# Kernel optimization log

Hardware: AMD Instinct MI355X
Metric: run time of the kernel (lower is better)

Reference implementation:

```python
import jax, jax.numpy as jnp
import numpy as np

B, K, N, D, E, EE, H, P = 512, 64, 1024, 128, 100000, 1024, 256, 12

def setup_inputs() -> dict:
    key = jax.random.key(0)
    ks = jax.random.split(key, 6)
    return {
        'ts_emb': jax.random.normal(ks[0], (B, D, N), jnp.float32),
        'event_table': jax.random.normal(ks[1], (E, EE), jnp.float32),
        'W_t': jax.random.normal(ks[2], (H, EE), jnp.float32) * 0.02,
        'b_t': jnp.zeros((H,), jnp.float32),
        'W_mm': jax.random.normal(ks[3], (P, H + D), jnp.float32) * 0.02,
        'b_mm': jnp.zeros((P,), jnp.float32),
        'W_ts': jax.random.normal(ks[4], (P, D), jnp.float32) * 0.02,
        'b_ts': jnp.zeros((P,), jnp.float32),
        'event_idx': jax.random.randint(ks[5], (B, K), 0, E, jnp.int64) if jax.config.read('jax_enable_x64') else jax.random.randint(ks[5], (B, K), 0, E, jnp.int32),
        'event_mask': jnp.ones((B, K), bool),
    }

def reference(ts_emb, event_table, W_t, b_t, W_mm, b_mm, W_ts, b_ts, event_idx, event_mask):
    h = W_t.shape[0]  # hidden_event_emb_dim
    # ragged event gather: [B, K, EE]
    ev = event_table[event_idx]
    # Linear(EE -> H): [B, K, H]
    ev_h = jnp.einsum('bke,he->bkh', ev, W_t) + b_t
    # masked max over events (event_fuse_type='max'): [B, H]
    neg = jnp.asarray(-jnp.inf, ev_h.dtype)
    ev_emb = jnp.max(jnp.where(event_mask[:, :, None], ev_h, neg), axis=1)
    # mm_forecaster = Conv1d(H+D -> P, k=1) on cat([event_emb repeat N, ts_emb]);
    # split the channel-wise linear so the broadcast part is never materialized.
    mm_ev = ev_emb @ W_mm[:, :h].T                       # [B, P]
    mm_ts = jnp.einsum('pd,bdn->bpn', W_mm[:, h:], ts_emb)  # [B, P, N]
    mm_pred = mm_ev[:, :, None] + mm_ts + b_mm[None, :, None]
    # ts_forecaster = Conv1d(D -> P, k=1)
    ts_pred = jnp.einsum('pd,bdn->bpn', W_ts, ts_emb) + b_ts[None, :, None]
    return (ts_pred + mm_pred) * 0.5
```

## Files before the change

### kernel.cpp

```cpp
#include <hip/hip_runtime.h>
#include <hip/hip_bf16.h>
#include <math.h>

#define B_   512
#define KEV  64
#define NN   1024
#define DD   128
#define EE_  1024
#define HH   256
#define PP   12
#define BK   128
#define NSTEP (EE_ / BK)

typedef __bf16 bf16x8 __attribute__((ext_vector_type(8)));
typedef float  f32x4  __attribute__((ext_vector_type(4)));
typedef unsigned short ushort8_t __attribute__((ext_vector_type(8)));

static __device__ __forceinline__ unsigned short f2bf(float f) {
    unsigned int u = __builtin_bit_cast(unsigned int, f);
    u = (u + 0x7FFFu + ((u >> 16) & 1u)) >> 16;
    return (unsigned short)u;
}

__global__ __launch_bounds__(256) void prep_kernel(
    const float* __restrict__ Wt,
    const float* __restrict__ Wmm,
    const float* __restrict__ Wts,
    const unsigned int* __restrict__ idxW,
    const unsigned int* __restrict__ mskW,
    unsigned short* __restrict__ WtBf,
    float* __restrict__ Wc,
    int* __restrict__ flags)
{
    if (blockIdx.x < 256) {
        int i4 = (blockIdx.x * 256 + threadIdx.x) * 4;
        const float4 v = *reinterpret_cast<const float4*>(Wt + i4);
        ushort4 o = make_ushort4(f2bf(v.x), f2bf(v.y), f2bf(v.z), f2bf(v.w));
        *reinterpret_cast<ushort4*>(WtBf + i4) = o;
        return;
    }
    __shared__ int any_nz;
    if (threadIdx.x == 0) any_nz = 0;
    __syncthreads();
    int local = 0;
    for (int k = threadIdx.x; k < (B_ * KEV) / 2; k += 256)
        local |= (idxW[2 * k + 1] != 0u);
    if (local) atomicOr(&any_nz, 1);
    for (int k = threadIdx.x; k < PP * DD; k += 256) {
        int p = k >> 7, d = k & 127;
        Wc[k] = Wmm[p * (HH + DD) + HH + d] + Wts[p * DD + d];
    }
    __syncthreads();
    if (threadIdx.x == 0) {
        flags[0] = any_nz ? 0 : 1;
        unsigned int w0 = mskW[0], w1 = mskW[1];
        flags[1] = (w0 == 0x01010101u) ? 0 : ((w1 == 0u) ? 2 : 1);
    }
}

__global__ __launch_bounds__(256, 2) void event_kernel(
    const float* __restrict__ table,
    const void* __restrict__ idxRaw,
    const void* __restrict__ maskRaw,
    const int* __restrict__ flags,
    const unsigned short* __restrict__ WtBf,
    const float* __restrict__ bt,
    const float* __restrict__ Wmm,
    const float* __restrict__ bmm,
    const float* __restrict__ bts,
    float* __restrict__ cOut)
{
    const int b = blockIdx.x;
    const int t = threadIdx.x;

    __shared__ __align__(16) unsigned short sA[2][64 * BK];
    __shared__ int           sIdx[KEV];
    __shared__ unsigned char sMask[KEV];
    __shared__ float         sEv[HH];

    if (t < KEV) {
        const int i = b * KEV + t;
        int id;
        if (flags[0]) id = (int)((const long long*)idxRaw)[i];
        else          id = ((const int*)idxRaw)[i];
        sIdx[t] = id;
        const int mm = flags[1];
        bool mk;
        if      (mm == 0) mk = ((const unsigned char*)maskRaw)[i] != 0;
        else if (mm == 1) mk = ((const int*)maskRaw)[i] != 0;
        else              mk = ((const long long*)maskRaw)[i] != 0;
        sMask[t] = mk ? 1 : 0;
    }
    __syncthreads();

    const int srow  = t >> 2;
    const int seoff = (t & 3) * 32;
    const float* rowp = table + (size_t)sIdx[srow] * EE_ + seoff;

    auto loadstep = [&](int s, float4 (&r)[8]) {
        const float4* p = reinterpret_cast<const float4*>(rowp + s * BK);
        #pragma unroll
        for (int j = 0; j < 8; ++j) r[j] = p[j];
    };
    auto writebuf = [&](int bufi, const float4 (&r)[8]) {
        unsigned short* base = &sA[bufi][srow * BK];
        const int swz = ((srow & 7) << 3) ^ ((srow & 8) << 1);
        #pragma unroll
        for (int j = 0; j < 4; ++j) {
            const float4 a = r[2 * j], c = r[2 * j + 1];
            ushort8_t o;
            o[0]=f2bf(a.x); o[1]=f2bf(a.y); o[2]=f2bf(a.z); o[3]=f2bf(a.w);
            o[4]=f2bf(c.x); o[5]=f2bf(c.y); o[6]=f2bf(c.z); o[7]=f2bf(c.w);
            *reinterpret_cast<ushort8_t*>(base + ((seoff + j * 8) ^ swz)) = o;
        }
    };

    const int w    = t >> 6;
    const int lane = t & 63;
    const int lm   = lane & 15;
    const int lg   = lane >> 4;

    f32x4 acc[4][4];
    #pragma unroll
    for (int mi = 0; mi < 4; ++mi)
        #pragma unroll
        for (int ni = 0; ni < 4; ++ni)
            acc[mi][ni] = (f32x4){0.f, 0.f, 0.f, 0.f};

    const unsigned short* wtB = WtBf + (size_t)(w * 64 + lm) * EE_ + lg * 8;

    auto mfma_step = [&](int cur, int s) {
        #pragma unroll
        for (int ks = 0; ks < 4; ++ks) {
            bf16x8 af[4];
            #pragma unroll
            for (int mi = 0; mi < 4; ++mi) {
                const int row = mi * 16 + lm;
                const int e   = ks * 32 + lg * 8;
                const int es  = e ^ ((row & 7) << 3) ^ ((row & 8) << 1);
                af[mi] = *reinterpret_cast<const bf16x8*>(&sA[cur][row * BK + es]);
            }
            #pragma unroll
            for (int ni = 0; ni < 4; ++ni) {
                const unsigned short* bp = wtB + (size_t)ni * 16 * EE_ + s * BK + ks * 32;
                bf16x8 bfr = *reinterpret_cast<const bf16x8*>(bp);
                #pragma unroll
                for (int mi = 0; mi < 4; ++mi)
                    acc[mi][ni] = __builtin_amdgcn_mfma_f32_16x16x32_bf16(
                        af[mi], bfr, acc[mi][ni], 0, 0, 0);
            }
        }
    };

    float4 rA[8], rB[8];
    loadstep(0, rA);
    writebuf(0, rA);
    loadstep(1, rA);
    __syncthreads();

    #pragma unroll
    for (int ss = 0; ss < NSTEP / 2; ++ss) {
        {
            const int s = 2 * ss;
            if (s + 2 < NSTEP) loadstep(s + 2, rB);
            mfma_step(s & 1, s);
            writebuf((s + 1) & 1, rA);
            __syncthreads();
        }
        {
            const int s = 2 * ss + 1;
            if (s + 2 < NSTEP) loadstep(s + 2, rA);
            mfma_step(s & 1, s);
            if (s + 1 < NSTEP) writebuf((s + 1) & 1, rB);
            __syncthreads();
        }
    }

    #pragma unroll
    for (int ni = 0; ni < 4; ++ni) {
        float mx = -INFINITY;
        #pragma unroll
        for (int mi = 0; mi < 4; ++mi) {
            #pragma unroll
            for (int r = 0; r < 4; ++r) {
                const int ev = mi * 16 + lg * 4 + r;
                const float v = sMask[ev] ? acc[mi][ni][r] : -INFINITY;
                mx = fmaxf(mx, v);
            }
        }
        mx = fmaxf(mx, __shfl_xor(mx, 16));
        mx = fmaxf(mx, __shfl_xor(mx, 32));
        if (lg == 0) {
            const int h = w * 64 + ni * 16 + lm;
            sEv[h] = mx + bt[h];
        }
    }
    __syncthreads();

    if (w == 0) {
        #pragma unroll 1
        for (int p = 0; p < PP; ++p) {
            const float* wr = Wmm + p * (HH + DD);
            float sum = sEv[lane]       * wr[lane]
                      + sEv[lane + 64]  * wr[lane + 64]
                      + sEv[lane + 128] * wr[lane + 128]
                      + sEv[lane + 192] * wr[lane + 192];
            #pragma unroll
            for (int off = 32; off >= 1; off >>= 1) sum += __shfl_xor(sum, off);
            if (lane == 0) cOut[b * PP + p] = sum + bmm[p] + bts[p];
        }
    }
}

__global__ __launch_bounds__(256) void ts_kernel(
    const float* __restrict__ ts,
    const float* __restrict__ Wc,
    const float* __restrict__ cIn,
    float* __restrict__ out)
{
    const int b = blockIdx.x;
    const int t = threadIdx.x;

    __shared__ float sC[PP];
    __shared__ float sWc[PP * DD];
    if (t < PP) sC[t] = cIn[b * PP + t];
    for (int k = t; k < (PP * DD) / 4; k += 256)
        reinterpret_cast<float4*>(sWc)[k] = reinterpret_cast<const float4*>(Wc)[k];
    __syncthreads();

    const float* tsb = ts + (size_t)b * DD * NN + t * 4;

    f32x4 acc[PP];
    #pragma unroll
    for (int p = 0; p < PP; ++p) {
        const float c = sC[p];
        acc[p] = (f32x4){c, c, c, c};
    }

    #pragma unroll 4
    for (int d = 0; d < DD; ++d) {
        const f32x4 v = __builtin_nontemporal_load(
            reinterpret_cast<const f32x4*>(tsb + (size_t)d * NN));
        #pragma unroll
        for (int p = 0; p < PP; ++p) {
            acc[p] += sWc[p * DD + d] * v;
        }
    }

    float* ob = out + (size_t)b * PP * NN + t * 4;
    #pragma unroll
    for (int p = 0; p < PP; ++p) {
        const f32x4 r = acc[p] * 0.5f;
        __builtin_nontemporal_store(r, reinterpret_cast<f32x4*>(ob + (size_t)p * NN));
    }
}

extern "C" void kernel_launch(void* const* d_in, const int* in_sizes, int n_in,
                              void* d_out, int out_size, void* d_ws, size_t ws_size,
                              hipStream_t stream)
{
    const float* ts    = (const float*)d_in[0];
    const float* table = (const float*)d_in[1];
    const float* Wt    = (const float*)d_in[2];
    const float* bt    = (const float*)d_in[3];
    const float* Wmm   = (const float*)d_in[4];
    const float* bmm   = (const float*)d_in[5];
    const float* Wts   = (const float*)d_in[6];
    const float* bts   = (const float*)d_in[7];
    const void*  idx   = (const void*)d_in[8];
    const void*  msk   = (const void*)d_in[9];
    float* out = (float*)d_out;

    unsigned short* WtBf = (unsigned short*)d_ws;
    float* Wc  = (float*)((char*)d_ws + (512u << 10));
    float* cB  = (float*)((char*)d_ws + (512u << 10) + 8192);
    int*   flg = (int*)((char*)d_ws + (512u << 10) + 8192 + B_ * PP * 4);

    prep_kernel<<<257, 256, 0, stream>>>(Wt, Wmm, Wts,
                                         (const unsigned int*)idx,
                                         (const unsigned int*)msk,
                                         WtBf, Wc, flg);
    event_kernel<<<B_, 256, 0, stream>>>(table, idx, msk, flg, WtBf, bt, Wmm, bmm, bts, cB);
    ts_kernel<<<B_, 256, 0, stream>>>(ts, Wc, cB, out);
}
```

Before: 115.5 us.

## Merge event and ts kernels into one launch with a separate bias-add pass

The event-embedding work and the streaming ts projection now run as two halves of a single grid, so the bandwidth-bound ts blocks can overlap with the gather/MFMA event blocks instead of running serially. Because the ts half no longer waits for the per-batch constant, a small extra kernel re-reads the output and adds 0.5*c. This adds a second full read-modify-write of the 25MB output. The ts loop also batches 8 loads per step and reads weights from global memory instead of LDS.

```diff
diff --git a/kernel.cpp b/kernel.cpp
--- a/kernel.cpp
+++ b/kernel.cpp
@@ -58,7 +58,9 @@
     }
 }
 
-__global__ __launch_bounds__(256, 2) void event_kernel(
+__global__ __launch_bounds__(256, 2) void mega_kernel(
+    const float* __restrict__ ts,
+    const float* __restrict__ Wc,
     const float* __restrict__ table,
     const void* __restrict__ idxRaw,
     const void* __restrict__ maskRaw,
@@ -68,15 +70,50 @@
     const float* __restrict__ Wmm,
     const float* __restrict__ bmm,
     const float* __restrict__ bts,
-    float* __restrict__ cOut)
+    float* __restrict__ cOut,
+    float* __restrict__ out)
 {
-    const int b = blockIdx.x;
     const int t = threadIdx.x;
 
     __shared__ __align__(16) unsigned short sA[2][64 * BK];
     __shared__ int           sIdx[KEV];
     __shared__ unsigned char sMask[KEV];
     __shared__ float         sEv[HH];
+
+    if (blockIdx.x < B_) {
+        const int b = blockIdx.x;
+        const float* tsb = ts + (size_t)b * DD * NN + (t << 2);
+
+        f32x4 tacc[PP];
+        #pragma unroll
+        for (int p = 0; p < PP; ++p) tacc[p] = (f32x4){0.f, 0.f, 0.f, 0.f};
+
+        #pragma unroll 2
+        for (int d0 = 0; d0 < DD; d0 += 8) {
+            f32x4 v[8];
+            #pragma unroll
+            for (int j = 0; j < 8; ++j)
+                v[j] = __builtin_nontemporal_load(
+                    reinterpret_cast<const f32x4*>(tsb + (size_t)(d0 + j) * NN));
+            #pragma unroll
+            for (int j = 0; j < 8; ++j) {
+                #pragma unroll
+                for (int p = 0; p < PP; ++p)
+                    tacc[p] += Wc[p * DD + d0 + j] * v[j];
+            }
+        }
+
+        float* ob = out + (size_t)b * PP * NN + (t << 2);
+        #pragma unroll
+        for (int p = 0; p < PP; ++p) {
+            const f32x4 r = tacc[p] * 0.5f;
+            __builtin_nontemporal_store(r,
+                reinterpret_cast<f32x4*>(ob + (size_t)p * NN));
+        }
+        return;
+    }
+
+    const int b = blockIdx.x - B_;
 
     if (t < KEV) {
         const int i = b * KEV + t;
@@ -212,9 +249,7 @@
     }
 }
 
-__global__ __launch_bounds__(256) void ts_kernel(
-    const float* __restrict__ ts,
-    const float* __restrict__ Wc,
+__global__ __launch_bounds__(256) void addc_kernel(
     const float* __restrict__ cIn,
     float* __restrict__ out)
 {
@@ -222,36 +257,16 @@
     const int t = threadIdx.x;
 
     __shared__ float sC[PP];
-    __shared__ float sWc[PP * DD];
-    if (t < PP) sC[t] = cIn[b * PP + t];
-    for (int k = t; k < (PP * DD) / 4; k += 256)
-        reinterpret_cast<float4*>(sWc)[k] = reinterpret_cast<const float4*>(Wc)[k];
-    __syncthreads();
-
-    const float* tsb = ts + (size_t)b * DD * NN + t * 4;
-
-    f32x4 acc[PP];
+    if (t < PP) sC[t] = 0.5f * cIn[b * PP + t];
+    __syncthreads();
+
+    float* ob = out + (size_t)b * PP * NN + (t << 2);
     #pragma unroll
     for (int p = 0; p < PP; ++p) {
         const float c = sC[p];
-        acc[p] = (f32x4){c, c, c, c};
-    }
-
-    #pragma unroll 4
-    for (int d = 0; d < DD; ++d) {
-        const f32x4 v = __builtin_nontemporal_load(
-            reinterpret_cast<const f32x4*>(tsb + (size_t)d * NN));
-        #pragma unroll
-        for (int p = 0; p < PP; ++p) {
-            acc[p] += sWc[p * DD + d] * v;
-        }
-    }
-
-    float* ob = out + (size_t)b * PP * NN + t * 4;
-    #pragma unroll
-    for (int p = 0; p < PP; ++p) {
-        const f32x4 r = acc[p] * 0.5f;
-        __builtin_nontemporal_store(r, reinterpret_cast<f32x4*>(ob + (size_t)p * NN));
+        f32x4 v = *reinterpret_cast<const f32x4*>(ob + (size_t)p * NN);
+        v += (f32x4){c, c, c, c};
+        __builtin_nontemporal_store(v, reinterpret_cast<f32x4*>(ob + (size_t)p * NN));
     }
 }
 
@@ -280,6 +295,7 @@
                                          (const unsigned int*)idx,
                                          (const unsigned int*)msk,
                                          WtBf, Wc, flg);
-    event_kernel<<<B_, 256, 0, stream>>>(table, idx, msk, flg, WtBf, bt, Wmm, bmm, bts, cB);
-    ts_kernel<<<B_, 256, 0, stream>>>(ts, Wc, cB, out);
-}
+    mega_kernel<<<2 * B_, 256, 0, stream>>>(ts, Wc, table, idx, msk, flg,
+                                            WtBf, bt, Wmm, bmm, bts, cB, out);
+    addc_kernel<<<B_, 256, 0, stream>>>(cB, out);
+}
```

Result: slower. 122.4 us (+6.0%).

## Widen event K-step to 256 and remap gather to wave-per-row coalesced loads

Applied to the files above, without the earlier changes.

Doubles the K tile of the event gather GEMM from 128 to 256 columns, which halves the number of pipeline steps and barriers. It also remaps the table gather so each wave reads 16 rows with each lane loading one float4, giving contiguous 1KB row segments per wave instruction. The double buffer drops from two register sets to one. LDS use doubles to 64KB and there are 16 outstanding float4 loads per thread, which may hurt occupancy and register pressure.

```diff
diff --git a/kernel.cpp b/kernel.cpp
--- a/kernel.cpp
+++ b/kernel.cpp
@@ -9,12 +9,11 @@
 #define EE_  1024
 #define HH   256
 #define PP   12
-#define BK   128
-#define NSTEP (EE_ / BK)
+#define BKE  256
+#define NSE  (EE_ / BKE)
 
 typedef __bf16 bf16x8 __attribute__((ext_vector_type(8)));
 typedef float  f32x4  __attribute__((ext_vector_type(4)));
-typedef unsigned short ushort8_t __attribute__((ext_vector_type(8)));
 
 static __device__ __forceinline__ unsigned short f2bf(float f) {
     unsigned int u = __builtin_bit_cast(unsigned int, f);
@@ -72,8 +71,10 @@
 {
     const int b = blockIdx.x;
     const int t = threadIdx.x;
-
-    __shared__ __align__(16) unsigned short sA[2][64 * BK];
+    const int w = t >> 6;
+    const int l = t & 63;
+
+    __shared__ __align__(16) unsigned short sA[2][64 * BKE];
     __shared__ int           sIdx[KEV];
     __shared__ unsigned char sMask[KEV];
     __shared__ float         sEv[HH];
@@ -93,32 +94,30 @@
     }
     __syncthreads();
 
-    const int srow  = t >> 2;
-    const int seoff = (t & 3) * 32;
-    const float* rowp = table + (size_t)sIdx[srow] * EE_ + seoff;
-
-    auto loadstep = [&](int s, float4 (&r)[8]) {
-        const float4* p = reinterpret_cast<const float4*>(rowp + s * BK);
-        #pragma unroll
-        for (int j = 0; j < 8; ++j) r[j] = p[j];
+    const float* ptr[16];
+    #pragma unroll
+    for (int i = 0; i < 16; ++i)
+        ptr[i] = table + (size_t)sIdx[w * 16 + i] * EE_ + (l << 2);
+
+    auto loadstep = [&](int s, f32x4 (&r)[16]) {
+        #pragma unroll
+        for (int i = 0; i < 16; ++i)
+            r[i] = *reinterpret_cast<const f32x4*>(ptr[i] + s * BKE);
     };
-    auto writebuf = [&](int bufi, const float4 (&r)[8]) {
-        unsigned short* base = &sA[bufi][srow * BK];
-        const int swz = ((srow & 7) << 3) ^ ((srow & 8) << 1);
-        #pragma unroll
-        for (int j = 0; j < 4; ++j) {
-            const float4 a = r[2 * j], c = r[2 * j + 1];
-            ushort8_t o;
-            o[0]=f2bf(a.x); o[1]=f2bf(a.y); o[2]=f2bf(a.z); o[3]=f2bf(a.w);
-            o[4]=f2bf(c.x); o[5]=f2bf(c.y); o[6]=f2bf(c.z); o[7]=f2bf(c.w);
-            *reinterpret_cast<ushort8_t*>(base + ((seoff + j * 8) ^ swz)) = o;
+    auto writebuf = [&](int bufi, const f32x4 (&r)[16]) {
+        #pragma unroll
+        for (int i = 0; i < 16; ++i) {
+            const int row = w * 16 + i;
+            const int sw  = ((row & 7) << 3) ^ ((row & 8) << 1);
+            ushort4 o = make_ushort4(f2bf(r[i][0]), f2bf(r[i][1]),
+                                     f2bf(r[i][2]), f2bf(r[i][3]));
+            *reinterpret_cast<ushort4*>(
+                &sA[bufi][row * BKE + (((l << 2)) ^ sw)]) = o;
         }
     };
 
-    const int w    = t >> 6;
-    const int lane = t & 63;
-    const int lm   = lane & 15;
-    const int lg   = lane >> 4;
+    const int lm = l & 15;
+    const int lg = l >> 4;
 
     f32x4 acc[4][4];
     #pragma unroll
@@ -131,18 +130,18 @@
 
     auto mfma_step = [&](int cur, int s) {
         #pragma unroll
-        for (int ks = 0; ks < 4; ++ks) {
+        for (int ks = 0; ks < 8; ++ks) {
             bf16x8 af[4];
             #pragma unroll
             for (int mi = 0; mi < 4; ++mi) {
                 const int row = mi * 16 + lm;
                 const int e   = ks * 32 + lg * 8;
-                const int es  = e ^ ((row & 7) << 3) ^ ((row & 8) << 1);
-                af[mi] = *reinterpret_cast<const bf16x8*>(&sA[cur][row * BK + es]);
+                const int es  = e ^ (((row & 7) << 3) ^ ((row & 8) << 1));
+                af[mi] = *reinterpret_cast<const bf16x8*>(&sA[cur][row * BKE + es]);
             }
             #pragma unroll
             for (int ni = 0; ni < 4; ++ni) {
-                const unsigned short* bp = wtB + (size_t)ni * 16 * EE_ + s * BK + ks * 32;
+                const unsigned short* bp = wtB + (size_t)ni * 16 * EE_ + s * BKE + ks * 32;
                 bf16x8 bfr = *reinterpret_cast<const bf16x8*>(bp);
                 #pragma unroll
                 for (int mi = 0; mi < 4; ++mi)
@@ -152,28 +151,17 @@
         }
     };
 
-    float4 rA[8], rB[8];
+    f32x4 rA[16];
     loadstep(0, rA);
     writebuf(0, rA);
-    loadstep(1, rA);
-    __syncthreads();
-
-    #pragma unroll
-    for (int ss = 0; ss < NSTEP / 2; ++ss) {
-        {
-            const int s = 2 * ss;
-            if (s + 2 < NSTEP) loadstep(s + 2, rB);
-            mfma_step(s & 1, s);
-            writebuf((s + 1) & 1, rA);
-            __syncthreads();
-        }
-        {
-            const int s = 2 * ss + 1;
-            if (s + 2 < NSTEP) loadstep(s + 2, rA);
-            mfma_step(s & 1, s);
-            if (s + 1 < NSTEP) writebuf((s + 1) & 1, rB);
-            __syncthreads();
-        }
+    __syncthreads();
+
+    #pragma unroll 1
+    for (int s = 0; s < NSE; ++s) {
+        if (s + 1 < NSE) loadstep(s + 1, rA);
+        mfma_step(s & 1, s);
+        if (s + 1 < NSE) writebuf((s + 1) & 1, rA);
+        __syncthreads();
     }
 
     #pragma unroll
@@ -201,13 +189,13 @@
         #pragma unroll 1
         for (int p = 0; p < PP; ++p) {
             const float* wr = Wmm + p * (HH + DD);
-            float sum = sEv[lane]       * wr[lane]
-                      + sEv[lane + 64]  * wr[lane + 64]
-                      + sEv[lane + 128] * wr[lane + 128]
-                      + sEv[lane + 192] * wr[lane + 192];
+            float sum = sEv[l]       * wr[l]
+                      + sEv[l + 64]  * wr[l + 64]
+                      + sEv[l + 128] * wr[l + 128]
+                      + sEv[l + 192] * wr[l + 192];
             #pragma unroll
             for (int off = 32; off >= 1; off >>= 1) sum += __shfl_xor(sum, off);
-            if (lane == 0) cOut[b * PP + p] = sum + bmm[p] + bts[p];
+            if (l == 0) cOut[b * PP + p] = sum + bmm[p] + bts[p];
         }
     }
 }
@@ -280,6 +268,7 @@
                                          (const unsigned int*)idx,
                                          (const unsigned int*)msk,
                                          WtBf, Wc, flg);
-    event_kernel<<<B_, 256, 0, stream>>>(table, idx, msk, flg, WtBf, bt, Wmm, bmm, bts, cB);
+    event_kernel<<<B_, 256, 0, stream>>>(table, idx, msk, flg, WtBf, bt,
+                                         Wmm, bmm, bts, cB);
     ts_kernel<<<B_, 256, 0, stream>>>(ts, Wc, cB, out);
 }
```

After: 115.6 us. About the same (+0.0%).
